# Kernel optimization log

Hardware: AMD Instinct MI355X
Metric: run time of the kernel (lower is better)

The kernel has to match this reference:

```python
import jax, jax.numpy as jnp
import numpy as np

EMBED_DIM = 768
NUM_HEADS = 12
HEAD_DIM = EMBED_DIM // NUM_HEADS
MEMORY_SIZE = 64
B, T = 8, 1024


def setup_inputs() -> dict:
    key = jax.random.key(0)
    ks = jax.random.split(key, 8)
    s = 0.02
    return {
        "x": jax.random.normal(ks[0], (B, T, EMBED_DIM), dtype=jnp.float32),
        "w_qkv": jax.random.normal(ks[1], (EMBED_DIM, 3 * EMBED_DIM), dtype=jnp.float32) * s,
        "b_qkv": jax.random.normal(ks[2], (3 * EMBED_DIM,), dtype=jnp.float32) * s,
        "w_out": jax.random.normal(ks[3], (EMBED_DIM, EMBED_DIM), dtype=jnp.float32) * s,
        "b_out": jax.random.normal(ks[4], (EMBED_DIM,), dtype=jnp.float32) * s,
        "w_mem": jax.random.normal(ks[5], (EMBED_DIM, EMBED_DIM), dtype=jnp.float32) * s,
        "b_mem": jax.random.normal(ks[6], (EMBED_DIM,), dtype=jnp.float32) * s,
        "memory": jax.random.normal(ks[7], (1, MEMORY_SIZE, EMBED_DIM), dtype=jnp.float32),
    }


def reference(x, w_qkv, b_qkv, w_out, b_out, w_mem, b_mem, memory):
    Bx, Tx, C = x.shape
    H, D = NUM_HEADS, HEAD_DIM
    scale = 1.0 / np.sqrt(D).astype(np.float32)

    # qkv projection -> (3, B, H, T, D)
    qkv = (x @ w_qkv + b_qkv).reshape(Bx, Tx, 3, H, D)
    qkv = jnp.transpose(qkv, (2, 0, 3, 1, 4))
    q, k, v = qkv[0], qkv[1], qkv[2]

    # full (non-causal) local attention over T
    scores = jnp.einsum("bhqd,bhkd->bhqk", q, k) * scale  # (B,H,T,T)
    local_out = jnp.einsum("bhqk,bhkd->bhqd", jax.nn.softmax(scores, axis=-1), v)

    # memory attention: projected memory serves as both K and V
    mem = memory @ w_mem + b_mem                      # (1, M, C)
    mem = jnp.broadcast_to(mem, (Bx, MEMORY_SIZE, C))
    mem_kv = jnp.transpose(mem.reshape(Bx, MEMORY_SIZE, H, D), (0, 2, 1, 3))  # (B,H,M,D)
    mem_scores = jnp.einsum("bhqd,bhmd->bhqm", q, mem_kv) * scale
    mem_out = jnp.einsum("bhqm,bhmd->bhqd", jax.nn.softmax(mem_scores, axis=-1), mem_kv)

    out = (local_out + mem_out).transpose(0, 2, 1, 3).reshape(Bx, Tx, C)
    return out @ w_out + b_out
```

## Files before the change

### kernel.cpp

```cpp
#include <hip/hip_runtime.h>

#define EMBED 768
#define NH 12
#define HD 64
#define MEMN 64
#define BB 8
#define TT 1024
#define ROWS 8192
#define QKV_N 2304
#define QSZ 6291456

typedef short bf16x8_t __attribute__((ext_vector_type(8)));
typedef float f32x4_t __attribute__((ext_vector_type(4)));

__device__ __forceinline__ unsigned short f2b(float f){
    union { float f; unsigned int i; } v; v.f = f;
    unsigned int x = v.i;
    unsigned int r = x + 0x7fffu + ((x >> 16) & 1u);
    return (unsigned short)(r >> 16);
}
__device__ __forceinline__ unsigned short f2b_ru(float f){
    union { float f; unsigned int i; } v; v.f = f;
    return (unsigned short)((v.i + 0x8000u) >> 16);
}

__device__ __forceinline__ void gl16(const unsigned short* g, unsigned short* l){
    __builtin_amdgcn_global_load_lds(
        (const __attribute__((address_space(1))) void*)g,
        (__attribute__((address_space(3))) void*)l,
        16, 0, 0);
}

#define PREP_CVT   3072
#define PREP_TQKV  4800
#define PREP_TOUT  5376
#define PREP_TOTAL 5388

__global__ __launch_bounds__(256) void prep_kernel(
    const float* __restrict__ x,
    const float* __restrict__ w_qkv,
    const float* __restrict__ w_out,
    const float* __restrict__ memory,
    const float* __restrict__ w_mem,
    const float* __restrict__ b_mem,
    unsigned short* __restrict__ xb,
    unsigned short* __restrict__ wqkvT,
    unsigned short* __restrict__ woutT,
    unsigned short* __restrict__ mem_k,
    unsigned short* __restrict__ mem_v)
{
    __shared__ unsigned short pool[5120];
    const int bid = blockIdx.x;
    const int t = threadIdx.x;

    if (bid < PREP_CVT) {
        int i = bid * 2048 + t * 8;
        float4 f0 = *(const float4*)&x[i];
        float4 f1 = *(const float4*)&x[i + 4];
        union { bf16x8_t v; unsigned short s[8]; } u;
        u.s[0] = f2b(f0.x); u.s[1] = f2b(f0.y); u.s[2] = f2b(f0.z); u.s[3] = f2b(f0.w);
        u.s[4] = f2b(f1.x); u.s[5] = f2b(f1.y); u.s[6] = f2b(f1.z); u.s[7] = f2b(f1.w);
        *(bf16x8_t*)&xb[i] = u.v;
    } else if (bid < PREP_TOUT) {
        const float* in; unsigned short* out; int R, C, loc;
        if (bid < PREP_TQKV) { in = w_qkv; out = wqkvT; R = EMBED; C = QKV_N; loc = bid - PREP_CVT; }
        else                 { in = w_out; out = woutT; R = EMBED; C = EMBED; loc = bid - PREP_TQKV; }
        int nbc = C / 32;
        int bc = (loc % nbc) * 32, br = (loc / nbc) * 32;
        unsigned short (*tile)[33] = (unsigned short(*)[33])pool;
        int lr = t >> 5, lc = t & 31;
        for (int i = 0; i < 4; i++) {
            int r = lr + i * 8;
            tile[r][lc] = f2b(in[(size_t)(br + r) * C + bc + lc]);
        }
        __syncthreads();
        for (int i = 0; i < 4; i++) {
            int r = lr + i * 8;
            out[(size_t)(bc + r) * R + br + lc] = tile[lc][r];
        }
    } else {
        unsigned short (*As)[40] = (unsigned short(*)[40])pool;
        unsigned short (*Bs)[40] = (unsigned short(*)[40])(pool + 2560);
        int wave = t >> 6, lane = t & 63;
        int ln = lane & 15, lq = lane >> 4;
        int bn = (bid - PREP_TOUT) * 64;
        const int K = EMBED, N = EMBED;

        f32x4_t acc[4];
        for (int i = 0; i < 4; i++) acc[i] = (f32x4_t)(0.f);
        int sm = t >> 2, sk = (t & 3) * 8;
        int bk = t >> 3, bn8 = (t & 7) * 8;

        for (int k0 = 0; k0 < K; k0 += 32) {
            __syncthreads();
            {
                float4 f0 = *(const float4*)&memory[(size_t)sm * K + k0 + sk];
                float4 f1 = *(const float4*)&memory[(size_t)sm * K + k0 + sk + 4];
                unsigned short* ap = &As[sm][sk];
                ap[0] = f2b(f0.x); ap[1] = f2b(f0.y); ap[2] = f2b(f0.z); ap[3] = f2b(f0.w);
                ap[4] = f2b(f1.x); ap[5] = f2b(f1.y); ap[6] = f2b(f1.z); ap[7] = f2b(f1.w);
            }
            {
                float4 g0 = *(const float4*)&w_mem[(size_t)(k0 + bk) * N + bn + bn8];
                float4 g1 = *(const float4*)&w_mem[(size_t)(k0 + bk) * N + bn + bn8 + 4];
                Bs[bn8 + 0][bk] = f2b(g0.x); Bs[bn8 + 1][bk] = f2b(g0.y);
                Bs[bn8 + 2][bk] = f2b(g0.z); Bs[bn8 + 3][bk] = f2b(g0.w);
                Bs[bn8 + 4][bk] = f2b(g1.x); Bs[bn8 + 5][bk] = f2b(g1.y);
                Bs[bn8 + 6][bk] = f2b(g1.z); Bs[bn8 + 7][bk] = f2b(g1.w);
            }
            __syncthreads();
            bf16x8_t a = *(bf16x8_t*)&As[wave * 16 + ln][lq * 8];
            for (int nt = 0; nt < 4; nt++) {
                bf16x8_t bf = *(bf16x8_t*)&Bs[nt * 16 + ln][lq * 8];
                acc[nt] = __builtin_amdgcn_mfma_f32_16x16x32_bf16(a, bf, acc[nt], 0, 0, 0);
            }
        }
        for (int nt = 0; nt < 4; nt++) {
            int c = bn + nt * 16 + ln;
            float bv = b_mem[c];
            for (int r = 0; r < 4; r++) {
                int row = wave * 16 + lq * 4 + r;
                int h = c >> 6, d = c & 63;
                unsigned short o = f2b(acc[nt][r] + bv);
                mem_k[((h * 64 + row) << 6) + d] = o;
                mem_v[((h * 64 + d) << 6) + row] = o;
            }
        }
    }
}

__global__ __launch_bounds__(256) void vtrans_kernel(
    const unsigned short* __restrict__ in, unsigned short* __restrict__ out)
{
    __shared__ unsigned short tile[64][72];
    int t0 = blockIdx.x * 64;
    int bh = blockIdx.y;
    const unsigned short* ip = in + ((size_t)bh * TT + t0) * 64;
    unsigned short* op = out + ((size_t)bh * 64) * TT + t0;
    int t = threadIdx.x;
    for (int i = 0; i < 2; i++) {
        int idx = i * 256 + t;
        int r = idx >> 3, c8 = (idx & 7) * 8;
        *(bf16x8_t*)&tile[r][c8] = *(const bf16x8_t*)&ip[(size_t)r * 64 + c8];
    }
    __syncthreads();
    for (int i = 0; i < 2; i++) {
        int idx = i * 256 + t;
        int d = idx >> 3, tc8 = (idx & 7) * 8;
        union { bf16x8_t v; unsigned short s[8]; } u;
        for (int j = 0; j < 8; j++) u.s[j] = tile[tc8 + j][d];
        *(bf16x8_t*)&op[(size_t)d * TT + tc8] = u.v;
    }
}

__global__ __launch_bounds__(256) void gemm_bt(
    const unsigned short* __restrict__ A,
    const unsigned short* __restrict__ BT,
    const float* __restrict__ bias,
    unsigned short* __restrict__ dq,
    unsigned short* __restrict__ dkv,
    float* __restrict__ df,
    int M, int N, int K, int mode)
{
    __shared__ unsigned short As[8192];
    __shared__ unsigned short Bs[8192];
    const int t = threadIdx.x;
    const int wave = t >> 6, lane = t & 63;
    const int ln = lane & 15, lq = lane >> 4;
    const int wm = (wave >> 1) * 64, wn = (wave & 1) * 64;
    const int bm = blockIdx.y * 128, bn = blockIdx.x * 128;

    f32x4_t acc[4][4];
    for (int i = 0; i < 4; i++)
        for (int j = 0; j < 4; j++) acc[i][j] = (f32x4_t)(0.f);

    const int rl8 = lane >> 3;
    const int swz = ((lane & 7) ^ rl8) * 8;
    const unsigned short* Ap = A + (size_t)(bm + wave * 32 + rl8) * K + swz;
    const unsigned short* Bp = BT + (size_t)(bn + wave * 32 + rl8) * K + swz;
    unsigned short* asd = &As[wave * 2048];
    unsigned short* bsd = &Bs[wave * 2048];

    const int e0 = (lq ^ (ln & 7)) * 8;
    const int e1 = e0 ^ 32;

    for (int k0 = 0; k0 < K; k0 += 64) {
        __syncthreads();
        for (int i = 0; i < 4; i++) {
            gl16(Ap + (size_t)(i * 8) * K + k0, asd + i * 512);
            gl16(Bp + (size_t)(i * 8) * K + k0, bsd + i * 512);
        }
        __syncthreads();

        {
            bf16x8_t af[4], bfr[4];
            for (int mt = 0; mt < 4; mt++)
                af[mt] = *(bf16x8_t*)&As[(wm + mt * 16 + ln) * 64 + e0];
            for (int nt = 0; nt < 4; nt++)
                bfr[nt] = *(bf16x8_t*)&Bs[(wn + nt * 16 + ln) * 64 + e0];
            for (int mt = 0; mt < 4; mt++)
                for (int nt = 0; nt < 4; nt++)
                    acc[mt][nt] = __builtin_amdgcn_mfma_f32_16x16x32_bf16(
                        af[mt], bfr[nt], acc[mt][nt], 0, 0, 0);
        }
        {
            bf16x8_t af[4], bfr[4];
            for (int mt = 0; mt < 4; mt++)
                af[mt] = *(bf16x8_t*)&As[(wm + mt * 16 + ln) * 64 + e1];
            for (int nt = 0; nt < 4; nt++)
                bfr[nt] = *(bf16x8_t*)&Bs[(wn + nt * 16 + ln) * 64 + e1];
            for (int mt = 0; mt < 4; mt++)
                for (int nt = 0; nt < 4; nt++)
                    acc[mt][nt] = __builtin_amdgcn_mfma_f32_16x16x32_bf16(
                        af[mt], bfr[nt], acc[mt][nt], 0, 0, 0);
        }
    }

    const float QSCALE = 0.125f * 1.44269504088896340736f;
    if (mode == 0) {
        const int s = bn / 768;
        for (int nt = 0; nt < 4; nt++) {
            int c = bn + wn + nt * 16 + ln;
            int rem = c - s * 768;
            int h = rem >> 6, d = rem & 63;
            float bv = bias[c];
            for (int mt = 0; mt < 4; mt++) {
                for (int r = 0; r < 4; r++) {
                    int row = bm + wm + mt * 16 + lq * 4 + r;
                    float val = acc[mt][nt][r] + bv;
                    if (s == 0) {
                        dq[(size_t)row * 768 + rem] = f2b(val * QSCALE);
                    } else {
                        int bb = row >> 10, tt = row & 1023;
                        dkv[(size_t)(s - 1) * QSZ +
                            (((size_t)(bb * 12 + h) * 1024 + tt) << 6) + d] = f2b(val);
                    }
                }
            }
        }
    } else {
        for (int nt = 0; nt < 4; nt++) {
            int c = bn + wn + nt * 16 + ln;
            float bv = bias[c];
            for (int mt = 0; mt < 4; mt++)
                for (int r = 0; r < 4; r++) {
                    int row = bm + wm + mt * 16 + lq * 4 + r;
                    df[(size_t)row * N + c] = acc[mt][nt][r] + bv;
                }
        }
    }
}

__global__ __launch_bounds__(256) void attn_kernel(
    unsigned short* __restrict__ qio,
    const unsigned short* __restrict__ k_ws,
    const unsigned short* __restrict__ vT_ws,
    const unsigned short* __restrict__ mem_k,
    const unsigned short* __restrict__ mem_v)
{
    __shared__ unsigned short Qs[4096];
    __shared__ unsigned short Ks[8192];
    __shared__ unsigned short Vs[8192];
    unsigned short* Ps = Qs;

    const int t = threadIdx.x;
    const int wave = t >> 6, lane = t & 63;
    const int ln = lane & 15, lq = lane >> 4;
    const int rl = lane >> 3;
    const int cl = ((lane & 7) ^ rl) * 8;

    int bid = blockIdx.x;
    int xcd = bid & 7, rest = bid >> 3;
    int bh = xcd * 12 + (rest >> 4);
    int qt = rest & 15;
    int b = bh / 12, h = bh - b * 12;

    unsigned short* qp = qio + ((size_t)(b * TT + qt * 64)) * 768 + h * 64;
    const unsigned short* kp = k_ws + (size_t)bh * TT * 64;
    const unsigned short* vp = vT_ws + ((size_t)bh << 16);
    const unsigned short* mkp = mem_k + h * 4096;
    const unsigned short* mvp = mem_v + h * 4096;

    {
        const unsigned short* qg = qp + (size_t)(wave * 8 + rl) * 768 + cl;
        gl16(qg, &Qs[wave * 512]);
        gl16(qg + (size_t)32 * 768, &Qs[2048 + wave * 512]);
    }
    __syncthreads();
    const int e0 = (lq ^ (ln & 7)) * 8;
    const int e1 = ((lq ^ (ln & 7)) ^ 4) * 8;
    bf16x8_t aq0 = *(bf16x8_t*)&Qs[(wave * 16 + ln) * 64 + e0];
    bf16x8_t aq1 = *(bf16x8_t*)&Qs[(wave * 16 + ln) * 64 + e1];

    const unsigned short* kg = kp + (wave * 8 + rl) * 64 + cl;
    const unsigned short* vg = vp + (size_t)(wave * 8 + rl) * 1024 + cl;

    const int hi3 = ln >> 3, lo3 = ln & 7;
    const int pm = (lq & 1) << 2;
    const int pw0 = (wave * 16 + lq * 4) * 64 + lo3;

    float lsum[4] = {0.f, 0.f, 0.f, 0.f};
    f32x4_t accO[4];
    for (int nt = 0; nt < 4; nt++) accO[nt] = (f32x4_t)(0.f);

    for (int kt = 0; kt < 8; kt++) {
        __syncthreads();
        gl16(kg + kt * 8192,        &Ks[wave * 512]);
        gl16(kg + kt * 8192 + 2048, &Ks[2048 + wave * 512]);
        gl16(kg + kt * 8192 + 4096, &Ks[4096 + wave * 512]);
        gl16(kg + kt * 8192 + 6144, &Ks[6144 + wave * 512]);
        gl16(vg + kt * 128,                       &Vs[wave * 512]);
        gl16(vg + (size_t)32 * 1024 + kt * 128,      &Vs[2048 + wave * 512]);
        gl16(vg + kt * 128 + 64,                  &Vs[4096 + wave * 512]);
        gl16(vg + (size_t)32 * 1024 + kt * 128 + 64, &Vs[6144 + wave * 512]);
        __syncthreads();

        for (int half = 0; half < 2; half++) {
            const unsigned short* Kh = &Ks[half * 4096];
            const unsigned short* Vh = &Vs[half * 4096];
            f32x4_t s[4];
            for (int nt = 0; nt < 4; nt++) s[nt] = (f32x4_t)(0.f);
            for (int nt = 0; nt < 4; nt++)
                s[nt] = __builtin_amdgcn_mfma_f32_16x16x32_bf16(
                    aq0, *(bf16x8_t*)&Kh[(nt * 16 + ln) * 64 + e0], s[nt], 0, 0, 0);
            for (int nt = 0; nt < 4; nt++)
                s[nt] = __builtin_amdgcn_mfma_f32_16x16x32_bf16(
                    aq1, *(bf16x8_t*)&Kh[(nt * 16 + ln) * 64 + e1], s[nt], 0, 0, 0);

            for (int nt = 0; nt < 4; nt++) {
                for (int r = 0; r < 4; r++) {
                    float p = __builtin_amdgcn_exp2f(s[nt][r]);
                    lsum[r] += p;
                    int chp = (nt * 2 + hi3) ^ pm ^ r;
                    Ps[pw0 + r * 64 + chp * 8] = f2b_ru(p);
                }
            }
            bf16x8_t a0 = *(bf16x8_t*)&Ps[(wave * 16 + ln) * 64 + e0];
            bf16x8_t a1 = *(bf16x8_t*)&Ps[(wave * 16 + ln) * 64 + e1];
            for (int nt = 0; nt < 4; nt++) {
                accO[nt] = __builtin_amdgcn_mfma_f32_16x16x32_bf16(
                    a0, *(bf16x8_t*)&Vh[(nt * 16 + ln) * 64 + e0], accO[nt], 0, 0, 0);
                accO[nt] = __builtin_amdgcn_mfma_f32_16x16x32_bf16(
                    a1, *(bf16x8_t*)&Vh[(nt * 16 + ln) * 64 + e1], accO[nt], 0, 0, 0);
            }
        }
    }

    __syncthreads();
    {
        const unsigned short* mk = mkp + (wave * 8 + rl) * 64 + cl;
        const unsigned short* mv = mvp + (wave * 8 + rl) * 64 + cl;
        gl16(mk, &Ks[wave * 512]);
        gl16(mk + 2048, &Ks[2048 + wave * 512]);
        gl16(mv, &Vs[wave * 512]);
        gl16(mv + 2048, &Vs[2048 + wave * 512]);
    }
    __syncthreads();

    f32x4_t s2[4];
    for (int nt = 0; nt < 4; nt++) s2[nt] = (f32x4_t)(0.f);
    for (int nt = 0; nt < 4; nt++)
        s2[nt] = __builtin_amdgcn_mfma_f32_16x16x32_bf16(
            aq0, *(bf16x8_t*)&Ks[(nt * 16 + ln) * 64 + e0], s2[nt], 0, 0, 0);
    for (int nt = 0; nt < 4; nt++)
        s2[nt] = __builtin_amdgcn_mfma_f32_16x16x32_bf16(
            aq1, *(bf16x8_t*)&Ks[(nt * 16 + ln) * 64 + e1], s2[nt], 0, 0, 0);

    float l2[4] = {0.f, 0.f, 0.f, 0.f};
    for (int nt = 0; nt < 4; nt++) {
        for (int r = 0; r < 4; r++) {
            float p = __builtin_amdgcn_exp2f(s2[nt][r]);
            l2[r] += p;
            int chp = (nt * 2 + hi3) ^ pm ^ r;
            Ps[pw0 + r * 64 + chp * 8] = f2b_ru(p);
        }
    }
    f32x4_t accM[4];
    for (int nt = 0; nt < 4; nt++) accM[nt] = (f32x4_t)(0.f);
    {
        bf16x8_t a0 = *(bf16x8_t*)&Ps[(wave * 16 + ln) * 64 + e0];
        bf16x8_t a1 = *(bf16x8_t*)&Ps[(wave * 16 + ln) * 64 + e1];
        for (int nt = 0; nt < 4; nt++) {
            accM[nt] = __builtin_amdgcn_mfma_f32_16x16x32_bf16(
                a0, *(bf16x8_t*)&Vs[(nt * 16 + ln) * 64 + e0], accM[nt], 0, 0, 0);
            accM[nt] = __builtin_amdgcn_mfma_f32_16x16x32_bf16(
                a1, *(bf16x8_t*)&Vs[(nt * 16 + ln) * 64 + e1], accM[nt], 0, 0, 0);
        }
    }

    float inv[4], inv2[4];
    for (int r = 0; r < 4; r++) {
        float a = lsum[r], c = l2[r];
        a += __shfl_xor(a, 1); a += __shfl_xor(a, 2);
        a += __shfl_xor(a, 4); a += __shfl_xor(a, 8);
        c += __shfl_xor(c, 1); c += __shfl_xor(c, 2);
        c += __shfl_xor(c, 4); c += __shfl_xor(c, 8);
        inv[r] = 1.f / a;
        inv2[r] = 1.f / c;
    }

    for (int nt = 0; nt < 4; nt++) {
        for (int r = 0; r < 4; r++) {
            int lrow = wave * 16 + lq * 4 + r;
            int lcol = nt * 16 + ln;
            float val = accO[nt][r] * inv[r] + accM[nt][r] * inv2[r];
            qp[(size_t)lrow * 768 + lcol] = f2b(val);
        }
    }
}

extern "C" void kernel_launch(void* const* d_in, const int* in_sizes, int n_in,
                              void* d_out, int out_size, void* d_ws, size_t ws_size,
                              hipStream_t stream) {
    const float* x      = (const float*)d_in[0];
    const float* w_qkv  = (const float*)d_in[1];
    const float* b_qkv  = (const float*)d_in[2];
    const float* w_out  = (const float*)d_in[3];
    const float* b_out  = (const float*)d_in[4];
    const float* w_mem  = (const float*)d_in[5];
    const float* b_mem  = (const float*)d_in[6];
    const float* memory = (const float*)d_in[7];

    unsigned short* ws = (unsigned short*)d_ws;
    unsigned short* q_ws   = ws;
    unsigned short* k_ws   = ws + (size_t)QSZ;
    unsigned short* woutT  = ws + 3 * (size_t)QSZ;
    unsigned short* mem_k  = woutT + (size_t)EMBED * EMBED;
    unsigned short* mem_v  = mem_k + (size_t)NH * MEMN * HD;

    unsigned short* xb    = (unsigned short*)d_out;
    unsigned short* wqkvT = xb + (size_t)QSZ;
    unsigned short* vT    = (unsigned short*)d_out;

    prep_kernel<<<PREP_TOTAL, 256, 0, stream>>>(
        x, w_qkv, w_out, memory, w_mem, b_mem, xb, wqkvT, woutT, mem_k, mem_v);

    gemm_bt<<<dim3(QKV_N / 128, ROWS / 128), 256, 0, stream>>>(
        xb, wqkvT, b_qkv, q_ws, k_ws, nullptr, ROWS, QKV_N, EMBED, 0);

    vtrans_kernel<<<dim3(TT / 64, BB * NH), 256, 0, stream>>>(k_ws + (size_t)QSZ, vT);

    attn_kernel<<<16 * NH * BB, 256, 0, stream>>>(q_ws, k_ws, vT, mem_k, mem_v);

    gemm_bt<<<dim3(EMBED / 128, ROWS / 128), 256, 0, stream>>>(
        q_ws, woutT, b_out, nullptr, nullptr, (float*)d_out, ROWS, EMBED, EMBED, 1);
}
```

Baseline: 254.5 us.

## Use 512-thread blocks for QKV GEMM and attention to share K/V tiles

Adds a dedicated 512-thread QKV GEMM kernel that computes 256x128 output tiles, so each B tile loaded into shared memory serves twice as many rows. The attention kernel likewise moves to 512 threads handling 128 query rows per block, halving the number of times each head's K/V tiles are fetched from global memory. The output GEMM keeps the old 256-thread path with the mode branch removed. In exchange, per-block shared memory rises and the attention grid drops to 768 blocks, which could reduce occupancy or latency hiding.

After: 241.2 us. -5.2%, faster.

```diff
diff --git a/kernel.cpp b/kernel.cpp
--- a/kernel.cpp
+++ b/kernel.cpp
@@ -153,14 +153,97 @@
     }
 }
 
-__global__ __launch_bounds__(256) void gemm_bt(
+__global__ __launch_bounds__(512) void gemm512(
     const unsigned short* __restrict__ A,
     const unsigned short* __restrict__ BT,
     const float* __restrict__ bias,
     unsigned short* __restrict__ dq,
     unsigned short* __restrict__ dkv,
+    int M, int N, int K)
+{
+    __shared__ unsigned short As[16384];
+    __shared__ unsigned short Bs[8192];
+    const int t = threadIdx.x;
+    const int wave = t >> 6, lane = t & 63;
+    const int ln = lane & 15, lq = lane >> 4;
+    const int wm = (wave >> 1) * 64, wn = (wave & 1) * 64;
+    const int bm = blockIdx.y * 256, bn = blockIdx.x * 128;
+
+    f32x4_t acc[4][4];
+    for (int i = 0; i < 4; i++)
+        for (int j = 0; j < 4; j++) acc[i][j] = (f32x4_t)(0.f);
+
+    const int rl8 = lane >> 3;
+    const int swz = ((lane & 7) ^ rl8) * 8;
+    const unsigned short* Ap = A + (size_t)(bm + wave * 32 + rl8) * K + swz;
+    const unsigned short* Bp = BT + (size_t)(bn + wave * 16 + rl8) * K + swz;
+    unsigned short* asd = &As[wave * 2048];
+    unsigned short* bsd = &Bs[wave * 1024];
+
+    const int e0 = (lq ^ (ln & 7)) * 8;
+    const int e1 = e0 ^ 32;
+
+    for (int k0 = 0; k0 < K; k0 += 64) {
+        __syncthreads();
+        for (int i = 0; i < 4; i++)
+            gl16(Ap + (size_t)(i * 8) * K + k0, asd + i * 512);
+        for (int i = 0; i < 2; i++)
+            gl16(Bp + (size_t)(i * 8) * K + k0, bsd + i * 512);
+        __syncthreads();
+
+        {
+            bf16x8_t af[4], bfr[4];
+            for (int mt = 0; mt < 4; mt++)
+                af[mt] = *(bf16x8_t*)&As[(wm + mt * 16 + ln) * 64 + e0];
+            for (int nt = 0; nt < 4; nt++)
+                bfr[nt] = *(bf16x8_t*)&Bs[(wn + nt * 16 + ln) * 64 + e0];
+            for (int mt = 0; mt < 4; mt++)
+                for (int nt = 0; nt < 4; nt++)
+                    acc[mt][nt] = __builtin_amdgcn_mfma_f32_16x16x32_bf16(
+                        af[mt], bfr[nt], acc[mt][nt], 0, 0, 0);
+        }
+        {
+            bf16x8_t af[4], bfr[4];
+            for (int mt = 0; mt < 4; mt++)
+                af[mt] = *(bf16x8_t*)&As[(wm + mt * 16 + ln) * 64 + e1];
+            for (int nt = 0; nt < 4; nt++)
+                bfr[nt] = *(bf16x8_t*)&Bs[(wn + nt * 16 + ln) * 64 + e1];
+            for (int mt = 0; mt < 4; mt++)
+                for (int nt = 0; nt < 4; nt++)
+                    acc[mt][nt] = __builtin_amdgcn_mfma_f32_16x16x32_bf16(
+                        af[mt], bfr[nt], acc[mt][nt], 0, 0, 0);
+        }
+    }
+
+    const float QSCALE = 0.125f * 1.44269504088896340736f;
+    const int s = bn / 768;
+    for (int nt = 0; nt < 4; nt++) {
+        int c = bn + wn + nt * 16 + ln;
+        int rem = c - s * 768;
+        int h = rem >> 6, d = rem & 63;
+        float bv = bias[c];
+        for (int mt = 0; mt < 4; mt++) {
+            for (int r = 0; r < 4; r++) {
+                int row = bm + wm + mt * 16 + lq * 4 + r;
+                float val = acc[mt][nt][r] + bv;
+                if (s == 0) {
+                    dq[(size_t)row * 768 + rem] = f2b(val * QSCALE);
+                } else {
+                    int bb = row >> 10, tt = row & 1023;
+                    dkv[(size_t)(s - 1) * QSZ +
+                        (((size_t)(bb * 12 + h) * 1024 + tt) << 6) + d] = f2b(val);
+                }
+            }
+        }
+    }
+}
+
+__global__ __launch_bounds__(256) void gemm_bt(
+    const unsigned short* __restrict__ A,
+    const unsigned short* __restrict__ BT,
+    const float* __restrict__ bias,
     float* __restrict__ df,
-    int M, int N, int K, int mode)
+    int M, int N, int K)
 {
     __shared__ unsigned short As[8192];
     __shared__ unsigned short Bs[8192];
@@ -216,49 +299,25 @@
         }
     }
 
-    const float QSCALE = 0.125f * 1.44269504088896340736f;
-    if (mode == 0) {
-        const int s = bn / 768;
-        for (int nt = 0; nt < 4; nt++) {
-            int c = bn + wn + nt * 16 + ln;
-            int rem = c - s * 768;
-            int h = rem >> 6, d = rem & 63;
-            float bv = bias[c];
-            for (int mt = 0; mt < 4; mt++) {
-                for (int r = 0; r < 4; r++) {
-                    int row = bm + wm + mt * 16 + lq * 4 + r;
-                    float val = acc[mt][nt][r] + bv;
-                    if (s == 0) {
-                        dq[(size_t)row * 768 + rem] = f2b(val * QSCALE);
-                    } else {
-                        int bb = row >> 10, tt = row & 1023;
-                        dkv[(size_t)(s - 1) * QSZ +
-                            (((size_t)(bb * 12 + h) * 1024 + tt) << 6) + d] = f2b(val);
-                    }
-                }
-            }
-        }
-    } else {
-        for (int nt = 0; nt < 4; nt++) {
-            int c = bn + wn + nt * 16 + ln;
-            float bv = bias[c];
-            for (int mt = 0; mt < 4; mt++)
-                for (int r = 0; r < 4; r++) {
-                    int row = bm + wm + mt * 16 + lq * 4 + r;
-                    df[(size_t)row * N + c] = acc[mt][nt][r] + bv;
-                }
-        }
-    }
-}
-
-__global__ __launch_bounds__(256) void attn_kernel(
+    for (int nt = 0; nt < 4; nt++) {
+        int c = bn + wn + nt * 16 + ln;
+        float bv = bias[c];
+        for (int mt = 0; mt < 4; mt++)
+            for (int r = 0; r < 4; r++) {
+                int row = bm + wm + mt * 16 + lq * 4 + r;
+                df[(size_t)row * N + c] = acc[mt][nt][r] + bv;
+            }
+    }
+}
+
+__global__ __launch_bounds__(512) void attn_kernel(
     unsigned short* __restrict__ qio,
     const unsigned short* __restrict__ k_ws,
     const unsigned short* __restrict__ vT_ws,
     const unsigned short* __restrict__ mem_k,
     const unsigned short* __restrict__ mem_v)
 {
-    __shared__ unsigned short Qs[4096];
+    __shared__ unsigned short Qs[8192];
     __shared__ unsigned short Ks[8192];
     __shared__ unsigned short Vs[8192];
     unsigned short* Ps = Qs;
@@ -271,20 +330,20 @@
 
     int bid = blockIdx.x;
     int xcd = bid & 7, rest = bid >> 3;
-    int bh = xcd * 12 + (rest >> 4);
-    int qt = rest & 15;
+    int bh = xcd * 12 + (rest >> 3);
+    int qt = rest & 7;
     int b = bh / 12, h = bh - b * 12;
 
-    unsigned short* qp = qio + ((size_t)(b * TT + qt * 64)) * 768 + h * 64;
+    unsigned short* qp = qio + ((size_t)(b * TT + qt * 128)) * 768 + h * 64;
     const unsigned short* kp = k_ws + (size_t)bh * TT * 64;
     const unsigned short* vp = vT_ws + ((size_t)bh << 16);
     const unsigned short* mkp = mem_k + h * 4096;
     const unsigned short* mvp = mem_v + h * 4096;
 
     {
-        const unsigned short* qg = qp + (size_t)(wave * 8 + rl) * 768 + cl;
-        gl16(qg, &Qs[wave * 512]);
-        gl16(qg + (size_t)32 * 768, &Qs[2048 + wave * 512]);
+        const unsigned short* qg = qp + (size_t)(wave * 16 + rl) * 768 + cl;
+        gl16(qg, &Qs[wave * 1024]);
+        gl16(qg + (size_t)8 * 768, &Qs[wave * 1024 + 512]);
     }
     __syncthreads();
     const int e0 = (lq ^ (ln & 7)) * 8;
@@ -292,8 +351,8 @@
     bf16x8_t aq0 = *(bf16x8_t*)&Qs[(wave * 16 + ln) * 64 + e0];
     bf16x8_t aq1 = *(bf16x8_t*)&Qs[(wave * 16 + ln) * 64 + e1];
 
-    const unsigned short* kg = kp + (wave * 8 + rl) * 64 + cl;
-    const unsigned short* vg = vp + (size_t)(wave * 8 + rl) * 1024 + cl;
+    const unsigned short* kg = kp + (wave * 16 + rl) * 64 + cl;
+    const unsigned short* vg = vp + (size_t)((wave & 3) * 16 + rl) * 1024 + (wave >> 2) * 64 + cl;
 
     const int hi3 = ln >> 3, lo3 = ln & 7;
     const int pm = (lq & 1) << 2;
@@ -305,14 +364,10 @@
 
     for (int kt = 0; kt < 8; kt++) {
         __syncthreads();
-        gl16(kg + kt * 8192,        &Ks[wave * 512]);
-        gl16(kg + kt * 8192 + 2048, &Ks[2048 + wave * 512]);
-        gl16(kg + kt * 8192 + 4096, &Ks[4096 + wave * 512]);
-        gl16(kg + kt * 8192 + 6144, &Ks[6144 + wave * 512]);
-        gl16(vg + kt * 128,                       &Vs[wave * 512]);
-        gl16(vg + (size_t)32 * 1024 + kt * 128,      &Vs[2048 + wave * 512]);
-        gl16(vg + kt * 128 + 64,                  &Vs[4096 + wave * 512]);
-        gl16(vg + (size_t)32 * 1024 + kt * 128 + 64, &Vs[6144 + wave * 512]);
+        gl16(kg + kt * 8192,        &Ks[wave * 1024]);
+        gl16(kg + kt * 8192 + 512,  &Ks[wave * 1024 + 512]);
+        gl16(vg + kt * 128,                 &Vs[wave * 1024]);
+        gl16(vg + (size_t)8 * 1024 + kt * 128, &Vs[wave * 1024 + 512]);
         __syncthreads();
 
         for (int half = 0; half < 2; half++) {
@@ -347,14 +402,8 @@
     }
 
     __syncthreads();
-    {
-        const unsigned short* mk = mkp + (wave * 8 + rl) * 64 + cl;
-        const unsigned short* mv = mvp + (wave * 8 + rl) * 64 + cl;
-        gl16(mk, &Ks[wave * 512]);
-        gl16(mk + 2048, &Ks[2048 + wave * 512]);
-        gl16(mv, &Vs[wave * 512]);
-        gl16(mv + 2048, &Vs[2048 + wave * 512]);
-    }
+    gl16(mkp + (wave * 8 + rl) * 64 + cl, &Ks[wave * 512]);
+    gl16(mvp + (wave * 8 + rl) * 64 + cl, &Vs[wave * 512]);
     __syncthreads();
 
     f32x4_t s2[4];
@@ -435,13 +484,13 @@
     prep_kernel<<<PREP_TOTAL, 256, 0, stream>>>(
         x, w_qkv, w_out, memory, w_mem, b_mem, xb, wqkvT, woutT, mem_k, mem_v);
 
-    gemm_bt<<<dim3(QKV_N / 128, ROWS / 128), 256, 0, stream>>>(
-        xb, wqkvT, b_qkv, q_ws, k_ws, nullptr, ROWS, QKV_N, EMBED, 0);
+    gemm512<<<dim3(QKV_N / 128, ROWS / 256), 512, 0, stream>>>(
+        xb, wqkvT, b_qkv, q_ws, k_ws, ROWS, QKV_N, EMBED);
 
     vtrans_kernel<<<dim3(TT / 64, BB * NH), 256, 0, stream>>>(k_ws + (size_t)QSZ, vT);
 
-    attn_kernel<<<16 * NH * BB, 256, 0, stream>>>(q_ws, k_ws, vT, mem_k, mem_v);
+    attn_kernel<<<8 * NH * BB, 512, 0, stream>>>(q_ws, k_ws, vT, mem_k, mem_v);
 
     gemm_bt<<<dim3(EMBED / 128, ROWS / 128), 256, 0, stream>>>(
-        q_ws, woutT, b_out, nullptr, nullptr, (float*)d_out, ROWS, EMBED, EMBED, 1);
-}
+        q_ws, woutT, b_out, (float*)d_out, ROWS, EMBED, EMBED);
+}
```
